# Kernel tuning notes

Measured on AMD Instinct MI355X. Metric: run time of the kernel, lower is better.

The kernel has to match this reference:

```python
import jax, jax.numpy as jnp
import numpy as np

E = 23  # unique experts
K = 3   # activated experts per token


def setup_inputs() -> dict:
    key = jax.random.key(0)
    ks = jax.random.split(key, 8)
    B, S, D, H = 4, 1024, 1024, 768
    sd = 1.0 / np.sqrt(D)
    sh = 1.0 / np.sqrt(H)
    return {
        "x": jax.random.normal(ks[0], (B, S, D), jnp.float32),
        "gate_W": jax.random.normal(ks[1], (D, E), jnp.float32) * sd,
        "gate_b": jnp.zeros((E,), jnp.float32),
        "route_bias": jnp.zeros((E,), jnp.float32),  # registered buffer 'bias'
        "W1": jax.random.normal(ks[2], (E, D, H), jnp.float32) * sd,
        "b1": jnp.zeros((E, H), jnp.float32),
        "W2": jax.random.normal(ks[3], (E, H, D), jnp.float32) * sh,
        "b2": jnp.zeros((E, D), jnp.float32),
        "sW1": jax.random.normal(ks[4], (D, H), jnp.float32) * sd,
        "sb1": jnp.zeros((H,), jnp.float32),
        "sW2": jax.random.normal(ks[5], (H, D), jnp.float32) * sh,
        "sb2": jnp.zeros((D,), jnp.float32),
    }


def _gelu(x):
    return jax.nn.gelu(x, approximate=False)  # torch nn.GELU default = exact erf


def reference(x, gate_W, gate_b, route_bias, W1, b1, W2, b2, sW1, sb1, sW2, sb2):
    o_shape = x.shape
    xt = x.reshape(-1, o_shape[-1])                       # [N, D]
    N = xt.shape[0]
    gate_weights = jax.nn.sigmoid(xt @ gate_W + gate_b)   # [N, E]
    _, top_idx = jax.lax.top_k(gate_weights + route_bias, K)  # [N, K]
    top_w = jnp.take_along_axis(gate_weights, top_idx, axis=-1)
    top_w = top_w / top_w.sum(axis=-1, keepdims=True)     # [N, K]
    onehot = jax.nn.one_hot(top_idx, E, dtype=xt.dtype)   # [N, K, E]
    combine = jnp.einsum('nke,nk->ne', onehot, top_w)     # [N, E] routed weights
    counts = onehot.sum(axis=(0, 1))                      # tokens per expert
    # dense-equivalent grouped expert MLPs (same math as gather/split/concat)
    h = _gelu(jnp.einsum('nd,edh->enh', xt, W1) + b1[:, None, :])   # [E, N, H]
    y = jnp.einsum('enh,ehd->end', h, W2) + b2[:, None, :]          # [E, N, D]
    routed = jnp.einsum('end,ne->nd', y, combine)
    shared = _gelu(xt @ sW1 + sb1) @ sW2 + sb2
    out = shared + routed
    # aux load-balance loss
    gw_norm = gate_weights / gate_weights.sum(axis=-1, keepdims=True)
    P = gw_norm.mean(axis=0)
    Fvec = (E * counts) / (K * N)
    aux_loss = (P * Fvec).sum()
    return out.reshape(o_shape), aux_loss
```

## Files before the change

kernel.cpp:

```cpp
#include <hip/hip_runtime.h>
#include <hip/hip_bf16.h>
#include <stdint.h>

#define N_TOK 4096
#define DDIM  1024
#define HDIM  768
#define NEXP  23
#define TOPK  3
#define MAXTILE 152
#define SLOTS   19456
#define GATE_BLKS 256

typedef float floatx4 __attribute__((ext_vector_type(4)));
typedef short short8  __attribute__((ext_vector_type(8)));

__device__ __forceinline__ short f2bf(float f) {
    __hip_bfloat16 h = __float2bfloat16(f);
    return *reinterpret_cast<short*>(&h);
}
__device__ __forceinline__ float bf2f(short s) {
    unsigned u = ((unsigned)(unsigned short)s) << 16;
    return __uint_as_float(u);
}
__device__ __forceinline__ float gelu_erf(float v) {
    return 0.5f * v * (1.0f + erff(v * 0.70710678118654752f));
}
__device__ __forceinline__ void gl_lds16(const short* g, short* l) {
    __builtin_amdgcn_global_load_lds(
        (const __attribute__((address_space(1))) void*)g,
        (__attribute__((address_space(3))) void*)l, 16, 0, 0);
}

__global__ __launch_bounds__(256) void gate_kernel(
    const float* __restrict__ x, const float* __restrict__ gate_W,
    const float* __restrict__ gate_b, const float* __restrict__ route_bias,
    int* __restrict__ top_idx, float* __restrict__ top_w,
    float* __restrict__ psum_part)
{
    __shared__ float gw[512 * NEXP];
    __shared__ float ps[4][NEXP];
    const int t = threadIdx.x;
    const int wave = t >> 6, lane = t & 63;
    const int n0 = blockIdx.x * 16 + wave * 4;

    float acc[4][NEXP];
#pragma unroll
    for (int k = 0; k < 4; k++)
#pragma unroll
        for (int e = 0; e < NEXP; e++) acc[k][e] = 0.f;

    for (int ph = 0; ph < 2; ph++) {
        if (ph) __syncthreads();
        {
            const float2* src = (const float2*)gate_W + ph * (512 * NEXP / 2);
            float2* dst = (float2*)gw;
            for (int i = t; i < 512 * NEXP / 2; i += 256) dst[i] = src[i];
        }
        __syncthreads();
#pragma unroll
        for (int c = 0; c < 8; c++) {
            const int d = ph * 512 + c * 64 + lane;
            float xd[4];
#pragma unroll
            for (int k = 0; k < 4; k++) xd[k] = x[(size_t)(n0 + k) * DDIM + d];
            const float* wrow = gw + (c * 64 + lane) * NEXP;
#pragma unroll
            for (int e = 0; e < NEXP; e++) {
                const float wv = wrow[e];
#pragma unroll
                for (int k = 0; k < 4; k++) acc[k][e] = fmaf(xd[k], wv, acc[k][e]);
            }
        }
    }
    for (int off = 32; off > 0; off >>= 1)
#pragma unroll
        for (int k = 0; k < 4; k++)
#pragma unroll
            for (int e = 0; e < NEXP; e++)
                acc[k][e] += __shfl_xor(acc[k][e], off, 64);

    if (lane == 0) {
        float pw[NEXP];
#pragma unroll
        for (int e = 0; e < NEXP; e++) pw[e] = 0.f;
        for (int k = 0; k < 4; k++) {
            const int n = n0 + k;
            float p[NEXP], s = 0.f;
#pragma unroll
            for (int e = 0; e < NEXP; e++) {
                p[e] = 1.f / (1.f + expf(-(acc[k][e] + gate_b[e])));
                s += p[e];
            }
            const float inv = 1.f / s;
#pragma unroll
            for (int e = 0; e < NEXP; e++) pw[e] += p[e] * inv;
            int idx[TOPK]; float w[TOPK]; bool used[NEXP] = {};
            for (int kk = 0; kk < TOPK; kk++) {
                float best = -1e30f; int bi = 0;
                for (int e = 0; e < NEXP; e++) {
                    if (!used[e]) {
                        float sc = p[e] + route_bias[e];
                        if (sc > best) { best = sc; bi = e; }
                    }
                }
                used[bi] = true; idx[kk] = bi; w[kk] = p[bi];
            }
            float wsum = w[0] + w[1] + w[2];
            for (int kk = 0; kk < TOPK; kk++) {
                top_idx[n * TOPK + kk] = idx[kk];
                top_w[n * TOPK + kk]   = w[kk] / wsum;
            }
        }
#pragma unroll
        for (int e = 0; e < NEXP; e++) ps[wave][e] = pw[e];
    }
    __syncthreads();
    if (t < NEXP)
        psum_part[t * GATE_BLKS + blockIdx.x] =
            ps[0][t] + ps[1][t] + ps[2][t] + ps[3][t];
}

#define P2_TCVT 2304
#define P2_XCVT N_TOK
#define P2_BIAS 168
#define P2_GRID (1 + P2_TCVT + P2_XCVT + P2_BIAS)

__global__ __launch_bounds__(256, 2) void prep2_kernel(
    const float* __restrict__ x, short* __restrict__ xb,
    const float* __restrict__ b1, const float* __restrict__ sb1,
    const float* __restrict__ b2, const float* __restrict__ sb2,
    float* __restrict__ bias1_all, float* __restrict__ bias2_all,
    const float* __restrict__ W1, const float* __restrict__ sW1, short* __restrict__ W1T,
    const float* __restrict__ W2, const float* __restrict__ sW2, short* __restrict__ W2T,
    const int* __restrict__ top_idx, const float* __restrict__ psum_part,
    int* __restrict__ tile_e, int* __restrict__ tok_of_slot,
    int* __restrict__ slot_of_tok, float* __restrict__ out_aux)
{
    __shared__ int   cnt[NEXP];
    __shared__ float psum[NEXP];
    __shared__ int   tbase[NEXP + 1];
    __shared__ int   lcur[NEXP];
    const int b = blockIdx.x;
    const int t = threadIdx.x;

    if (b == 0) {
        if (t < NEXP) { cnt[t] = 0; psum[t] = 0.f; lcur[t] = 0; }
        __syncthreads();

        const int4* ti4 = (const int4*)top_idx;
        for (int i = t; i < N_TOK * TOPK / 4; i += 256) {
            int4 v = ti4[i];
            atomicAdd(&cnt[v.x], 1); atomicAdd(&cnt[v.y], 1);
            atomicAdd(&cnt[v.z], 1); atomicAdd(&cnt[v.w], 1);
        }
#pragma unroll
        for (int e = 0; e < NEXP; e++) {
            float v = psum_part[e * GATE_BLKS + t];
            for (int off = 32; off > 0; off >>= 1) v += __shfl_xor(v, off, 64);
            if ((t & 63) == 0) atomicAdd(&psum[e], v);
        }
        __syncthreads();

        if (t == 0) {
            int tb = 0; float aux = 0.f;
            for (int e = 0; e < NEXP; e++) {
                tbase[e] = tb;
                float P = psum[e] / (float)N_TOK;
                float F = (float)NEXP * (float)cnt[e] / ((float)TOPK * (float)N_TOK);
                aux += P * F;
                tb += (cnt[e] + 127) >> 7;
            }
            tbase[NEXP] = tb;
            *out_aux = aux;
        }
        __syncthreads();
        const int tr = tbase[NEXP];
        const int P  = tr << 7;
        for (int i = t; i < MAXTILE; i += 256) {
            int v = -1;
            if (i < tr) {
                for (int e = 0; e < NEXP; e++)
                    if (i >= tbase[e] && i < tbase[e + 1]) v = e;
            } else if (i < tr + N_TOK / 128) v = NEXP;
            tile_e[i] = v;
        }
        for (int i = t; i < N_TOK * TOPK; i += 256) {
            const int e = top_idx[i];
            const int pos = atomicAdd(&lcur[e], 1);
            const int slot = (tbase[e] << 7) + pos;
            const int n = i / 3, k = i - n * 3;
            tok_of_slot[slot] = n;
            slot_of_tok[n * 4 + k] = slot;
        }
        for (int n = t; n < N_TOK; n += 256) {
            tok_of_slot[P + n] = n;
            slot_of_tok[n * 4 + 3] = P + n;
        }
        return;
    }
    const int bb = b - 1;
    if (bb < P2_TCVT) {
        int idx = bb;
        const float* s; short* d; int R, C, rt, ct;
        if (idx < 24 * 48) {
            const int wz = idx / 48, rem = idx % 48;
            R = DDIM; C = HDIM;
            rt = (rem / 6) * 128; ct = (rem % 6) * 128;
            s = (wz < NEXP) ? W1 + (size_t)wz * DDIM * HDIM : sW1;
            d = W1T + (size_t)wz * DDIM * HDIM;
        } else {
            idx -= 24 * 48;
            const int wz = idx / 48, rem = idx % 48;
            R = HDIM; C = DDIM;
            rt = (rem / 8) * 128; ct = (rem % 8) * 128;
            s = (wz < NEXP) ? W2 + (size_t)wz * HDIM * DDIM : sW2;
            d = W2T + (size_t)wz * HDIM * DDIM;
        }
        const int u = t & 15, q = t >> 4;
        const int r0 = rt + 8 * u, c0 = ct + 8 * q;
        float4 f[8][2];
#pragma unroll
        for (int i = 0; i < 8; i++) {
            f[i][0] = *(const float4*)&s[(size_t)(r0 + i) * C + c0];
            f[i][1] = *(const float4*)&s[(size_t)(r0 + i) * C + c0 + 4];
        }
#pragma unroll
        for (int j = 0; j < 8; j++) {
            const int hh = j >> 2, jj = j & 3;
            short8 col;
#pragma unroll
            for (int i = 0; i < 8; i++) {
                float v = (jj == 0) ? f[i][hh].x :
                          (jj == 1) ? f[i][hh].y :
                          (jj == 2) ? f[i][hh].z : f[i][hh].w;
                col[i] = f2bf(v);
            }
            *(short8*)&d[(size_t)(c0 + j) * R + r0] = col;
        }
    } else if (bb < P2_TCVT + P2_XCVT) {
        size_t i = (size_t)(bb - P2_TCVT) * 256 + t;
        float4 v = ((const float4*)x)[i];
        short4 o;
        o.x = f2bf(v.x); o.y = f2bf(v.y); o.z = f2bf(v.z); o.w = f2bf(v.w);
        ((short4*)xb)[i] = o;
    } else {
        int i = (bb - P2_TCVT - P2_XCVT) * 256 + t;
        if (i < 24 * HDIM) {
            bias1_all[i] = (i < NEXP * HDIM) ? b1[i] : sb1[i - NEXP * HDIM];
        } else {
            int j = i - 24 * HDIM;
            if (j < 24 * DDIM)
                bias2_all[j] = (j < NEXP * DDIM) ? b2[j] : sb2[j - NEXP * DDIM];
        }
    }
}

template <bool FFN1>
__global__ __launch_bounds__(256) void gemm_kernel(
    const short* __restrict__ Abase, const int* __restrict__ tok_of_slot,
    const int* __restrict__ tile_e, const short* __restrict__ Wall,
    const float* __restrict__ bias_all, short* __restrict__ outb)
{
    constexpr int KD = FFN1 ? DDIM : HDIM;
    constexpr int NC = FFN1 ? HDIM : DDIM;
    constexpr int KI = KD / 32;
    constexpr int GX = NC / 128;
    constexpr int NWG = GX * MAXTILE;
    constexpr int Q = NWG / 8, RM = NWG % 8;

    int bid = blockIdx.y * GX + blockIdx.x;
    {
        const int xcd = bid & 7, off = bid >> 3;
        bid = (xcd < RM) ? (xcd * (Q + 1) + off)
                         : (RM * (Q + 1) + (xcd - RM) * Q + off);
    }
    const int tile = bid / GX;
    const int e = tile_e[tile];
    if (e < 0) return;
    const int slot0 = tile * 128;
    const int n0 = (bid - tile * GX) * 128;

    __shared__ short smem[3 * 4096 * 2];
    short* const As = smem;
    short* const Bs = smem + 3 * 4096;

    const int t = threadIdx.x;
    const int w = t >> 6, l = t & 63;
    const int quad = l >> 4, l16 = l & 15;
    const int wr = w >> 1, wc = w & 1;

    const int ra0 = w * 32 + (l >> 2);
    const int ra1 = ra0 + 16;
    const int ko  = (l & 3) << 3;

    const short *ap0, *ap1;
    if constexpr (FFN1) {
        int t0 = tok_of_slot[slot0 + ra0];
        int t1 = tok_of_slot[slot0 + ra1];
        t0 = ((unsigned)t0 < (unsigned)N_TOK) ? t0 : 0;
        t1 = ((unsigned)t1 < (unsigned)N_TOK) ? t1 : 0;
        ap0 = Abase + (size_t)t0 * KD + ko;
        ap1 = Abase + (size_t)t1 * KD + ko;
    } else {
        ap0 = Abase + (size_t)(slot0 + ra0) * KD + ko;
        ap1 = Abase + (size_t)(slot0 + ra1) * KD + ko;
    }
    const short* bbase = Wall + (size_t)e * NC * KD + (size_t)n0 * KD;
    const short* bp0 = bbase + (size_t)ra0 * KD + ko;
    const short* bp1 = bbase + (size_t)ra1 * KD + ko;

    const int ldo0 = (w * 32) * 32;
    const int ldo1 = (w * 32 + 16) * 32;

    floatx4 acc[4][4] = {};

#pragma unroll
    for (int p = 0; p < 3; p++) {
        gl_lds16(ap0, As + p * 4096 + ldo0); gl_lds16(ap1, As + p * 4096 + ldo1);
        gl_lds16(bp0, Bs + p * 4096 + ldo0); gl_lds16(bp1, Bs + p * 4096 + ldo1);
        ap0 += 32; ap1 += 32; bp0 += 32; bp1 += 32;
    }

#pragma unroll
    for (int k = 0; k < KI; k++) {
        if (k < KI - 2)       asm volatile("s_waitcnt vmcnt(8)" ::: "memory");
        else if (k == KI - 2) asm volatile("s_waitcnt vmcnt(4)" ::: "memory");
        else                  asm volatile("s_waitcnt vmcnt(0)" ::: "memory");
        asm volatile("s_barrier" ::: "memory");

        const int s = k % 3;
        short8 af[4], bf[4];
#pragma unroll
        for (int i = 0; i < 4; i++)
            af[i] = *(const short8*)(As + s * 4096 + (wr * 64 + i * 16 + l16) * 32 + quad * 8);
#pragma unroll
        for (int j = 0; j < 4; j++)
            bf[j] = *(const short8*)(Bs + s * 4096 + (wc * 64 + j * 16 + l16) * 32 + quad * 8);
#pragma unroll
        for (int i = 0; i < 4; i++)
#pragma unroll
            for (int j = 0; j < 4; j++)
                acc[i][j] = __builtin_amdgcn_mfma_f32_16x16x32_bf16(af[i], bf[j], acc[i][j], 0, 0, 0);

        asm volatile("s_waitcnt lgkmcnt(0)" ::: "memory");
        asm volatile("s_barrier" ::: "memory");
        if (k + 3 < KI) {
            gl_lds16(ap0, As + s * 4096 + ldo0); gl_lds16(ap1, As + s * 4096 + ldo1);
            gl_lds16(bp0, Bs + s * 4096 + ldo0); gl_lds16(bp1, Bs + s * 4096 + ldo1);
            ap0 += 32; ap1 += 32; bp0 += 32; bp1 += 32;
        }
    }

    short* const OT = smem;
    const int bias_off = e * NC + n0;
#pragma unroll
    for (int j = 0; j < 4; j++) {
        const int colL = wc * 64 + j * 16 + l16;
        const float bv = bias_all[bias_off + colL];
        const int cg = colL >> 3, wi = colL & 7;
#pragma unroll
        for (int i = 0; i < 4; i++)
#pragma unroll
            for (int r = 0; r < 4; r++) {
                const int rowL = wr * 64 + i * 16 + quad * 4 + r;
                float v = acc[i][j][r] + bv;
                if constexpr (FFN1) v = gelu_erf(v);
                OT[rowL * 128 + (((cg ^ ((rowL >> 2) & 3)) << 3) | wi)] = f2bf(v);
            }
    }
    __syncthreads();
#pragma unroll
    for (int p = 0; p < 8; p++) {
        const int rowL = p * 16 + (t >> 4);
        const int g = t & 15;
        const short8 v = *(const short8*)(OT + rowL * 128 + ((g ^ ((rowL >> 2) & 3)) << 3));
        *(short8*)&outb[(size_t)(slot0 + rowL) * NC + n0 + g * 8] = v;
    }
}

__global__ __launch_bounds__(256) void combine_kernel(
    const short* __restrict__ ybuf, const int* __restrict__ slot_of_tok,
    const float* __restrict__ top_w, float* __restrict__ out)
{
    const int n = blockIdx.x;
    const int c = threadIdx.x;
    const int s0 = slot_of_tok[n * 4 + 0];
    const int s1 = slot_of_tok[n * 4 + 1];
    const int s2 = slot_of_tok[n * 4 + 2];
    const int ss = slot_of_tok[n * 4 + 3];
    const float w0 = top_w[n * 3 + 0];
    const float w1 = top_w[n * 3 + 1];
    const float w2 = top_w[n * 3 + 2];

    short4 y0 = ((const short4*)(ybuf + (size_t)s0 * DDIM))[c];
    short4 y1 = ((const short4*)(ybuf + (size_t)s1 * DDIM))[c];
    short4 y2 = ((const short4*)(ybuf + (size_t)s2 * DDIM))[c];
    short4 ys = ((const short4*)(ybuf + (size_t)ss * DDIM))[c];

    float4 o;
    o.x = bf2f(ys.x) + w0 * bf2f(y0.x) + w1 * bf2f(y1.x) + w2 * bf2f(y2.x);
    o.y = bf2f(ys.y) + w0 * bf2f(y0.y) + w1 * bf2f(y1.y) + w2 * bf2f(y2.y);
    o.z = bf2f(ys.z) + w0 * bf2f(y0.z) + w1 * bf2f(y1.z) + w2 * bf2f(y2.z);
    o.w = bf2f(ys.w) + w0 * bf2f(y0.w) + w1 * bf2f(y1.w) + w2 * bf2f(y2.w);
    ((float4*)(out + (size_t)n * DDIM))[c] = o;
}

extern "C" void kernel_launch(void* const* d_in, const int* in_sizes, int n_in,
                              void* d_out, int out_size, void* d_ws, size_t ws_size,
                              hipStream_t stream)
{
    const float* x          = (const float*)d_in[0];
    const float* gate_W     = (const float*)d_in[1];
    const float* gate_b     = (const float*)d_in[2];
    const float* route_bias = (const float*)d_in[3];
    const float* W1         = (const float*)d_in[4];
    const float* b1         = (const float*)d_in[5];
    const float* W2         = (const float*)d_in[6];
    const float* b2         = (const float*)d_in[7];
    const float* sW1        = (const float*)d_in[8];
    const float* sb1        = (const float*)d_in[9];
    const float* sW2        = (const float*)d_in[10];
    const float* sb2        = (const float*)d_in[11];
    float* out = (float*)d_out;

    uint8_t* ws = (uint8_t*)d_ws;
    int*   top_idx   = (int*)(ws);
    float* top_w     = (float*)(ws + 49152);
    int*   tile_e    = (int*)(ws + 98688);
    float* psum_part = (float*)(ws + 99328);
    int*   tok_slot  = (int*)(ws + 193536);
    int*   slot_tok  = (int*)(ws + 271360);
    float* bias1_all = (float*)(ws + 336896);
    float* bias2_all = (float*)(ws + 410624);
    short* xb        = (short*)(ws + 512000);
    short* W1T       = (short*)(ws + 8902656);
    short* W2T       = (short*)(ws + 46651392);
    short* hbuf      = (short*)(ws + 84400128);
    short* ybuf      = (short*)(ws + 512000);

    gate_kernel<<<GATE_BLKS, 256, 0, stream>>>(
        x, gate_W, gate_b, route_bias, top_idx, top_w, psum_part);
    prep2_kernel<<<P2_GRID, 256, 0, stream>>>(
        x, xb, b1, sb1, b2, sb2, bias1_all, bias2_all,
        W1, sW1, W1T, W2, sW2, W2T,
        top_idx, psum_part, tile_e, tok_slot, slot_tok,
        out + (size_t)N_TOK * DDIM);

    gemm_kernel<true><<<dim3(HDIM / 128, MAXTILE), 256, 0, stream>>>(
        xb, tok_slot, tile_e, W1T, bias1_all, hbuf);
    gemm_kernel<false><<<dim3(DDIM / 128, MAXTILE), 256, 0, stream>>>(
        hbuf, tok_slot, tile_e, W2T, bias2_all, ybuf);
    combine_kernel<<<N_TOK, 256, 0, stream>>>(ybuf, slot_tok, top_w, out);
}
```

Before: 477.9 us.

## Fuse x-to-bf16 conversion into per-token gate kernel

```diff
diff --git a/kernel.cpp b/kernel.cpp
--- a/kernel.cpp
+++ b/kernel.cpp
@@ -9,7 +9,6 @@
 #define TOPK  3
 #define MAXTILE 152
 #define SLOTS   19456
-#define GATE_BLKS 256
 
 typedef float floatx4 __attribute__((ext_vector_type(4)));
 typedef short short8  __attribute__((ext_vector_type(8)));
@@ -31,102 +30,90 @@
         (__attribute__((address_space(3))) void*)l, 16, 0, 0);
 }
 
-__global__ __launch_bounds__(256) void gate_kernel(
+__global__ __launch_bounds__(256) void gx_kernel(
     const float* __restrict__ x, const float* __restrict__ gate_W,
     const float* __restrict__ gate_b, const float* __restrict__ route_bias,
     int* __restrict__ top_idx, float* __restrict__ top_w,
-    float* __restrict__ psum_part)
+    float* __restrict__ psum_part, short* __restrict__ xb)
 {
-    __shared__ float gw[512 * NEXP];
     __shared__ float ps[4][NEXP];
+    const int n = blockIdx.x;
     const int t = threadIdx.x;
-    const int wave = t >> 6, lane = t & 63;
-    const int n0 = blockIdx.x * 16 + wave * 4;
-
-    float acc[4][NEXP];
-#pragma unroll
-    for (int k = 0; k < 4; k++)
-#pragma unroll
-        for (int e = 0; e < NEXP; e++) acc[k][e] = 0.f;
-
-    for (int ph = 0; ph < 2; ph++) {
-        if (ph) __syncthreads();
-        {
-            const float2* src = (const float2*)gate_W + ph * (512 * NEXP / 2);
-            float2* dst = (float2*)gw;
-            for (int i = t; i < 512 * NEXP / 2; i += 256) dst[i] = src[i];
-        }
-        __syncthreads();
-#pragma unroll
-        for (int c = 0; c < 8; c++) {
-            const int d = ph * 512 + c * 64 + lane;
-            float xd[4];
-#pragma unroll
-            for (int k = 0; k < 4; k++) xd[k] = x[(size_t)(n0 + k) * DDIM + d];
-            const float* wrow = gw + (c * 64 + lane) * NEXP;
-#pragma unroll
+    const int wave = t >> 6;
+
+    const size_t i = (size_t)n * 256 + t;
+    const float4 v = ((const float4*)x)[i];
+    short4 o;
+    o.x = f2bf(v.x); o.y = f2bf(v.y); o.z = f2bf(v.z); o.w = f2bf(v.w);
+    ((short4*)xb)[i] = o;
+
+    const float4* wp = (const float4*)(gate_W + (size_t)t * 92);
+    float4 w4[23];
+#pragma unroll
+    for (int j = 0; j < 23; j++) w4[j] = wp[j];
+
+    float partial[NEXP];
+#pragma unroll
+    for (int e = 0; e < NEXP; e++) partial[e] = 0.f;
+    const float xv0 = v.x, xv1 = v.y, xv2 = v.z, xv3 = v.w;
+#pragma unroll
+    for (int r = 0; r < 4; r++) {
+        const float xr = (r == 0) ? xv0 : (r == 1) ? xv1 : (r == 2) ? xv2 : xv3;
+#pragma unroll
+        for (int e = 0; e < NEXP; e++) {
+            const int f = r * 23 + e;
+            const int fj = f >> 2, fc = f & 3;
+            const float wv = (fc == 0) ? w4[fj].x : (fc == 1) ? w4[fj].y
+                           : (fc == 2) ? w4[fj].z : w4[fj].w;
+            partial[e] = fmaf(xr, wv, partial[e]);
+        }
+    }
+    for (int off = 32; off > 0; off >>= 1)
+#pragma unroll
+        for (int e = 0; e < NEXP; e++)
+            partial[e] += __shfl_xor(partial[e], off, 64);
+    if ((t & 63) == 0)
+#pragma unroll
+        for (int e = 0; e < NEXP; e++) ps[wave][e] = partial[e];
+    __syncthreads();
+
+    if (t == 0) {
+        float p[NEXP], s = 0.f;
+#pragma unroll
+        for (int e = 0; e < NEXP; e++) {
+            const float logit = ((ps[0][e] + ps[1][e]) + (ps[2][e] + ps[3][e]))
+                                + gate_b[e];
+            p[e] = 1.f / (1.f + expf(-logit));
+            s += p[e];
+        }
+        const float inv = 1.f / s;
+#pragma unroll
+        for (int e = 0; e < NEXP; e++)
+            psum_part[(size_t)e * N_TOK + n] = p[e] * inv;
+        int idx[TOPK]; float w[TOPK]; bool used[NEXP] = {};
+        for (int k = 0; k < TOPK; k++) {
+            float best = -1e30f; int bi = 0;
             for (int e = 0; e < NEXP; e++) {
-                const float wv = wrow[e];
-#pragma unroll
-                for (int k = 0; k < 4; k++) acc[k][e] = fmaf(xd[k], wv, acc[k][e]);
+                if (!used[e]) {
+                    float sc = p[e] + route_bias[e];
+                    if (sc > best) { best = sc; bi = e; }
+                }
             }
-        }
-    }
-    for (int off = 32; off > 0; off >>= 1)
-#pragma unroll
-        for (int k = 0; k < 4; k++)
-#pragma unroll
-            for (int e = 0; e < NEXP; e++)
-                acc[k][e] += __shfl_xor(acc[k][e], off, 64);
-
-    if (lane == 0) {
-        float pw[NEXP];
-#pragma unroll
-        for (int e = 0; e < NEXP; e++) pw[e] = 0.f;
-        for (int k = 0; k < 4; k++) {
-            const int n = n0 + k;
-            float p[NEXP], s = 0.f;
-#pragma unroll
-            for (int e = 0; e < NEXP; e++) {
-                p[e] = 1.f / (1.f + expf(-(acc[k][e] + gate_b[e])));
-                s += p[e];
-            }
-            const float inv = 1.f / s;
-#pragma unroll
-            for (int e = 0; e < NEXP; e++) pw[e] += p[e] * inv;
-            int idx[TOPK]; float w[TOPK]; bool used[NEXP] = {};
-            for (int kk = 0; kk < TOPK; kk++) {
-                float best = -1e30f; int bi = 0;
-                for (int e = 0; e < NEXP; e++) {
-                    if (!used[e]) {
-                        float sc = p[e] + route_bias[e];
-                        if (sc > best) { best = sc; bi = e; }
-                    }
-                }
-                used[bi] = true; idx[kk] = bi; w[kk] = p[bi];
-            }
-            float wsum = w[0] + w[1] + w[2];
-            for (int kk = 0; kk < TOPK; kk++) {
-                top_idx[n * TOPK + kk] = idx[kk];
-                top_w[n * TOPK + kk]   = w[kk] / wsum;
-            }
-        }
-#pragma unroll
-        for (int e = 0; e < NEXP; e++) ps[wave][e] = pw[e];
-    }
-    __syncthreads();
-    if (t < NEXP)
-        psum_part[t * GATE_BLKS + blockIdx.x] =
-            ps[0][t] + ps[1][t] + ps[2][t] + ps[3][t];
+            used[bi] = true; idx[k] = bi; w[k] = p[bi];
+        }
+        float wsum = w[0] + w[1] + w[2];
+        for (int k = 0; k < TOPK; k++) {
+            top_idx[n * TOPK + k] = idx[k];
+            top_w[n * TOPK + k]   = w[k] / wsum;
+        }
+    }
 }
 
 #define P2_TCVT 2304
-#define P2_XCVT N_TOK
 #define P2_BIAS 168
-#define P2_GRID (1 + P2_TCVT + P2_XCVT + P2_BIAS)
+#define P2_GRID (1 + P2_TCVT + P2_BIAS)
 
 __global__ __launch_bounds__(256, 2) void prep2_kernel(
-    const float* __restrict__ x, short* __restrict__ xb,
     const float* __restrict__ b1, const float* __restrict__ sb1,
     const float* __restrict__ b2, const float* __restrict__ sb2,
     float* __restrict__ bias1_all, float* __restrict__ bias2_all,
@@ -155,7 +142,9 @@
         }
 #pragma unroll
         for (int e = 0; e < NEXP; e++) {
-            float v = psum_part[e * GATE_BLKS + t];
+            float v = 0.f;
+            for (int i = t; i < N_TOK; i += 256)
+                v += psum_part[(size_t)e * N_TOK + i];
             for (int off = 32; off > 0; off >>= 1) v += __shfl_xor(v, off, 64);
             if ((t & 63) == 0) atomicAdd(&psum[e], v);
         }
@@ -237,14 +226,8 @@
             }
             *(short8*)&d[(size_t)(c0 + j) * R + r0] = col;
         }
-    } else if (bb < P2_TCVT + P2_XCVT) {
-        size_t i = (size_t)(bb - P2_TCVT) * 256 + t;
-        float4 v = ((const float4*)x)[i];
-        short4 o;
-        o.x = f2bf(v.x); o.y = f2bf(v.y); o.z = f2bf(v.z); o.w = f2bf(v.w);
-        ((short4*)xb)[i] = o;
     } else {
-        int i = (bb - P2_TCVT - P2_XCVT) * 256 + t;
+        int i = (bb - P2_TCVT) * 256 + t;
         if (i < 24 * HDIM) {
             bias1_all[i] = (i < NEXP * HDIM) ? b1[i] : sb1[i - NEXP * HDIM];
         } else {
@@ -428,20 +411,20 @@
     float* top_w     = (float*)(ws + 49152);
     int*   tile_e    = (int*)(ws + 98688);
     float* psum_part = (float*)(ws + 99328);
-    int*   tok_slot  = (int*)(ws + 193536);
-    int*   slot_tok  = (int*)(ws + 271360);
-    float* bias1_all = (float*)(ws + 336896);
-    float* bias2_all = (float*)(ws + 410624);
-    short* xb        = (short*)(ws + 512000);
-    short* W1T       = (short*)(ws + 8902656);
-    short* W2T       = (short*)(ws + 46651392);
-    short* hbuf      = (short*)(ws + 84400128);
-    short* ybuf      = (short*)(ws + 512000);
-
-    gate_kernel<<<GATE_BLKS, 256, 0, stream>>>(
-        x, gate_W, gate_b, route_bias, top_idx, top_w, psum_part);
+    int*   tok_slot  = (int*)(ws + 476160);
+    int*   slot_tok  = (int*)(ws + 553984);
+    float* bias1_all = (float*)(ws + 619520);
+    float* bias2_all = (float*)(ws + 693248);
+    short* xb        = (short*)(ws + 791552);
+    short* W1T       = (short*)(ws + 9180160);
+    short* W2T       = (short*)(ws + 46928896);
+    short* hbuf      = (short*)(ws + 84677632);
+    short* ybuf      = (short*)(ws + 791552);
+
+    gx_kernel<<<N_TOK, 256, 0, stream>>>(
+        x, gate_W, gate_b, route_bias, top_idx, top_w, psum_part, xb);
     prep2_kernel<<<P2_GRID, 256, 0, stream>>>(
-        x, xb, b1, sb1, b2, sb2, bias1_all, bias2_all,
+        b1, sb1, b2, sb2, bias1_all, bias2_all,
         W1, sW1, W1T, W2, sW2, W2T,
         top_idx, psum_part, tile_e, tok_slot, slot_tok,
         out + (size_t)N_TOK * DDIM);
```

New measurement: 460.6 us. -3.6%, faster.
